# Kernel tuning notes

Measured on AMD Instinct MI355X. Metric: run time of the kernel, lower is better.

## Reference

```python
import jax, jax.numpy as jnp
import numpy as np

DIM = 128
BITS = 4
LEVELS_HALF = 2 ** (BITS - 1)  # 8
# MSE-optimal uniform quantizer step constant for a unit-mean-abs Laplace source,
# 4-bit (16 levels). (TurboQuantMSE dist='laplace')
LAPLACE_STEP_C = 0.456
EPS = 1e-8
SQRT_DIM = float(np.sqrt(DIM))


def fwht(x):
    """Normalized fast Walsh-Hadamard transform over the last dim (power of 2)."""
    n = x.shape[-1]
    orig = x.shape
    y = x
    h = 1
    while h < n:
        y = y.reshape(orig[:-1] + (n // (2 * h), 2, h))
        a, b = y[..., 0, :], y[..., 1, :]
        y = jnp.stack([a + b, a - b], axis=-2).reshape(orig)
        h *= 2
    return y * (1.0 / np.sqrt(n))


def setup_inputs() -> dict:
    key = jax.random.key(0)
    k1, k2 = jax.random.split(key)
    x = jax.random.normal(k1, (4, 32, 4096, DIM), dtype=jnp.float32)
    signs = jax.random.uniform(k2, (1, DIM), dtype=jnp.float32)  # thresholded to +/-1 inside reference
    return {"x": x, "signs": signs}


def reference(x, signs):
    # random-sign Hadamard rotation passes
    s = jnp.where(signs >= 0.5, 1.0, -1.0).astype(x.dtype)  # [P, D]
    n_passes = s.shape[0]
    r = x
    for p in range(n_passes):
        r = fwht(r * s[p])
    # per-vector norm, unit-RMS normalize
    norms = jnp.sqrt(jnp.sum(r * r, axis=-1, keepdims=True))          # [..., 1]
    u = r / (norms + EPS) * SQRT_DIM                                   # unit-RMS coeffs
    # MSE-optimal Laplace step (per-vector scale)
    scales = LAPLACE_STEP_C * jnp.mean(jnp.abs(u), axis=-1, keepdims=True)  # [..., 1]
    q = jnp.clip(jnp.round(u / (scales + EPS)), -LEVELS_HALF, LEVELS_HALF - 1)
    code = (q + LEVELS_HALF).astype(jnp.uint8)                         # [0, 15]
    # pack: two 4-bit codes per byte
    packed = code[..., 0::2] | (code[..., 1::2] << 4)                  # [..., D//2] uint8
    # ---- dequantize ----
    lo = (packed & 0xF).astype(x.dtype) - LEVELS_HALF
    hi = (packed >> 4).astype(x.dtype) - LEVELS_HALF
    qd = jnp.stack([lo, hi], axis=-1).reshape(packed.shape[:-1] + (DIM,))
    r_hat = qd * scales * (norms / SQRT_DIM)
    x_hat = r_hat
    for p in range(n_passes - 1, -1, -1):
        x_hat = fwht(x_hat) * s[p]   # inverse of (H . diag(s)) is diag(s) . H (H symmetric orthonormal)
    return x_hat
```

## Files before the change

kernel.cpp:

```cpp
#include <hip/hip_runtime.h>
#include <math.h>


#define DIM 128
#define INV_SQRT_DIM 0.08838834764831845f

template <int M>
__device__ __forceinline__ float swz_xor(float v) {
    int r = __builtin_amdgcn_ds_swizzle(__float_as_int(v), (M << 10) | 0x1F);
    return __int_as_float(r);
}

__device__ __forceinline__ float sflip(float v, unsigned sbits, int k) {
    unsigned m = ((sbits >> k) & 1u) << 31;
    return __int_as_float(__float_as_int(v) ^ m);
}

__device__ __forceinline__ void fwht_raw(float a[16], int lane) {
#pragma unroll
    for (int h = 1; h < 16; h <<= 1) {
#pragma unroll
        for (int i = 0; i < 16; ++i) {
            if (!(i & h)) {
                float u = a[i], w = a[i + h];
                a[i] = u + w;
                a[i + h] = u - w;
            }
        }
    }
    {
        const float sgn = (lane & 1) ? -1.0f : 1.0f;
#pragma unroll
        for (int i = 0; i < 16; ++i) { float b = swz_xor<1>(a[i]); a[i] = fmaf(sgn, a[i], b); }
    }
    {
        const float sgn = (lane & 2) ? -1.0f : 1.0f;
#pragma unroll
        for (int i = 0; i < 16; ++i) { float b = swz_xor<2>(a[i]); a[i] = fmaf(sgn, a[i], b); }
    }
    {
        const float sgn = (lane & 4) ? -1.0f : 1.0f;
#pragma unroll
        for (int i = 0; i < 16; ++i) { float b = swz_xor<4>(a[i]); a[i] = fmaf(sgn, a[i], b); }
    }
}

__global__ __launch_bounds__(256) void turboquant_kernel(
    const float* __restrict__ x, const float* __restrict__ signs,
    float* __restrict__ out, long long nrows) {
    const int lane = threadIdx.x & 63;
    const int j    = lane & 7;
    const int rsub = lane >> 3;

    unsigned sbits = 0;
#pragma unroll
    for (int k = 0; k < 4; ++k) {
        float4 sv = *reinterpret_cast<const float4*>(signs + k * 32 + j * 4);
        if (sv.x < 0.5f) sbits |= 1u << (k * 4 + 0);
        if (sv.y < 0.5f) sbits |= 1u << (k * 4 + 1);
        if (sv.z < 0.5f) sbits |= 1u << (k * 4 + 2);
        if (sv.w < 0.5f) sbits |= 1u << (k * 4 + 3);
    }

    const long long waves_total = (long long)gridDim.x * 4;
    const long long wid = (long long)blockIdx.x * 4 + (threadIdx.x >> 6);

    for (long long it = wid; it * 8 < nrows; it += waves_total) {
        const long long row = it * 8 + rsub;
        const float* rp = x + row * DIM + j * 4;

        float a[16];
#pragma unroll
        for (int k = 0; k < 4; ++k) {
            float4 v = *reinterpret_cast<const float4*>(rp + k * 32);
            a[k * 4 + 0] = sflip(v.x, sbits, k * 4 + 0);
            a[k * 4 + 1] = sflip(v.y, sbits, k * 4 + 1);
            a[k * 4 + 2] = sflip(v.z, sbits, k * 4 + 2);
            a[k * 4 + 3] = sflip(v.w, sbits, k * 4 + 3);
        }

        fwht_raw(a, lane);

        float ss = 0.0f, sa = 0.0f;
#pragma unroll
        for (int i = 0; i < 16; ++i) {
            ss = fmaf(a[i], a[i], ss);
            sa += fabsf(a[i]);
        }
        ss += swz_xor<1>(ss); sa += swz_xor<1>(sa);
        ss += swz_xor<2>(ss); sa += swz_xor<2>(sa);
        ss += swz_xor<4>(ss); sa += swz_xor<4>(sa);

        const float norm   = sqrtf(ss) * INV_SQRT_DIM;
        const float t      = norm + 1e-8f;
        const float scales = (0.456f / 128.0f) * sa / t;
        const float sden   = scales + 1e-8f;
        const float id     = 1.0f / (t * sden);
        const float ofac   = scales * norm * (1.0f / 128.0f);

#pragma unroll
        for (int i = 0; i < 16; ++i)
            a[i] = fminf(fmaxf(rintf(a[i] * id), -8.0f), 7.0f);

        fwht_raw(a, lane);

        float* op = out + row * DIM + j * 4;
#pragma unroll
        for (int k = 0; k < 4; ++k) {
            float4 o;
            o.x = sflip(a[k * 4 + 0] * ofac, sbits, k * 4 + 0);
            o.y = sflip(a[k * 4 + 1] * ofac, sbits, k * 4 + 1);
            o.z = sflip(a[k * 4 + 2] * ofac, sbits, k * 4 + 2);
            o.w = sflip(a[k * 4 + 3] * ofac, sbits, k * 4 + 3);
            *reinterpret_cast<float4*>(op + k * 32) = o;
        }
    }
}

extern "C" void kernel_launch(void* const* d_in, const int* in_sizes, int n_in,
                              void* d_out, int out_size, void* d_ws, size_t ws_size,
                              hipStream_t stream) {
    const float* x     = (const float*)d_in[0];
    const float* signs = (const float*)d_in[1];
    float* out = (float*)d_out;
    const long long nrows = (long long)in_sizes[0] / DIM;
    turboquant_kernel<<<2048, 256, 0, stream>>>(x, signs, out, nrows);
}
```

Baseline: 106.0 us.

## Prefetch next row tile in registers and use DPP for xor-1/xor-2 shuffles

Each wave now loads the next tile's input into registers before processing the current one, so global load latency overlaps with the FWHT and quantization math. The lane-xor exchanges at distances 1 and 2 move from ds_swizzle to DPP quad_perm moves, which skip the LDS crossbar path. The cost is extra VGPRs for the prefetch buffer, which may lower occupancy. The kernel is memory-bound at about 16M rows, so the overall gain is likely small.

```diff
diff --git a/kernel.cpp b/kernel.cpp
--- a/kernel.cpp
+++ b/kernel.cpp
@@ -5,9 +5,14 @@
 #define DIM 128
 #define INV_SQRT_DIM 0.08838834764831845f
 
-template <int M>
-__device__ __forceinline__ float swz_xor(float v) {
-    int r = __builtin_amdgcn_ds_swizzle(__float_as_int(v), (M << 10) | 0x1F);
+__device__ __forceinline__ float dpp_xor1(float v) {
+    return __int_as_float(__builtin_amdgcn_mov_dpp(__float_as_int(v), 0xB1, 0xF, 0xF, false));
+}
+__device__ __forceinline__ float dpp_xor2(float v) {
+    return __int_as_float(__builtin_amdgcn_mov_dpp(__float_as_int(v), 0x4E, 0xF, 0xF, false));
+}
+__device__ __forceinline__ float swz_xor4(float v) {
+    int r = __builtin_amdgcn_ds_swizzle(__float_as_int(v), (4 << 10) | 0x1F);
     return __int_as_float(r);
 }
 
@@ -31,17 +36,17 @@
     {
         const float sgn = (lane & 1) ? -1.0f : 1.0f;
 #pragma unroll
-        for (int i = 0; i < 16; ++i) { float b = swz_xor<1>(a[i]); a[i] = fmaf(sgn, a[i], b); }
+        for (int i = 0; i < 16; ++i) { float b = dpp_xor1(a[i]); a[i] = fmaf(sgn, a[i], b); }
     }
     {
         const float sgn = (lane & 2) ? -1.0f : 1.0f;
 #pragma unroll
-        for (int i = 0; i < 16; ++i) { float b = swz_xor<2>(a[i]); a[i] = fmaf(sgn, a[i], b); }
+        for (int i = 0; i < 16; ++i) { float b = dpp_xor2(a[i]); a[i] = fmaf(sgn, a[i], b); }
     }
     {
         const float sgn = (lane & 4) ? -1.0f : 1.0f;
 #pragma unroll
-        for (int i = 0; i < 16; ++i) { float b = swz_xor<4>(a[i]); a[i] = fmaf(sgn, a[i], b); }
+        for (int i = 0; i < 16; ++i) { float b = swz_xor4(a[i]); a[i] = fmaf(sgn, a[i], b); }
     }
 }
 
@@ -62,21 +67,35 @@
         if (sv.w < 0.5f) sbits |= 1u << (k * 4 + 3);
     }
 
+    const long long ntiles = nrows >> 3;
     const long long waves_total = (long long)gridDim.x * 4;
-    const long long wid = (long long)blockIdx.x * 4 + (threadIdx.x >> 6);
+    long long t = (long long)blockIdx.x * 4 + (threadIdx.x >> 6);
 
-    for (long long it = wid; it * 8 < nrows; it += waves_total) {
-        const long long row = it * 8 + rsub;
-        const float* rp = x + row * DIM + j * 4;
+    const long long lofs = (long long)rsub * DIM + j * 4;
+
+    float4 cur[4];
+    if (t < ntiles) {
+        const float* rp = x + t * (8 * DIM) + lofs;
+#pragma unroll
+        for (int k = 0; k < 4; ++k) cur[k] = *reinterpret_cast<const float4*>(rp + k * 32);
+    }
+
+    while (t < ntiles) {
+        const long long tn = t + waves_total;
+        float4 nxt[4] = {};
+        if (tn < ntiles) {
+            const float* rp = x + tn * (8 * DIM) + lofs;
+#pragma unroll
+            for (int k = 0; k < 4; ++k) nxt[k] = *reinterpret_cast<const float4*>(rp + k * 32);
+        }
 
         float a[16];
 #pragma unroll
         for (int k = 0; k < 4; ++k) {
-            float4 v = *reinterpret_cast<const float4*>(rp + k * 32);
-            a[k * 4 + 0] = sflip(v.x, sbits, k * 4 + 0);
-            a[k * 4 + 1] = sflip(v.y, sbits, k * 4 + 1);
-            a[k * 4 + 2] = sflip(v.z, sbits, k * 4 + 2);
-            a[k * 4 + 3] = sflip(v.w, sbits, k * 4 + 3);
+            a[k * 4 + 0] = sflip(cur[k].x, sbits, k * 4 + 0);
+            a[k * 4 + 1] = sflip(cur[k].y, sbits, k * 4 + 1);
+            a[k * 4 + 2] = sflip(cur[k].z, sbits, k * 4 + 2);
+            a[k * 4 + 3] = sflip(cur[k].w, sbits, k * 4 + 3);
         }
 
         fwht_raw(a, lane);
@@ -87,15 +106,15 @@
             ss = fmaf(a[i], a[i], ss);
             sa += fabsf(a[i]);
         }
-        ss += swz_xor<1>(ss); sa += swz_xor<1>(sa);
-        ss += swz_xor<2>(ss); sa += swz_xor<2>(sa);
-        ss += swz_xor<4>(ss); sa += swz_xor<4>(sa);
+        ss += dpp_xor1(ss); sa += dpp_xor1(sa);
+        ss += dpp_xor2(ss); sa += dpp_xor2(sa);
+        ss += swz_xor4(ss); sa += swz_xor4(sa);
 
         const float norm   = sqrtf(ss) * INV_SQRT_DIM;
-        const float t      = norm + 1e-8f;
-        const float scales = (0.456f / 128.0f) * sa / t;
+        const float tt     = norm + 1e-8f;
+        const float scales = (0.456f / 128.0f) * sa / tt;
         const float sden   = scales + 1e-8f;
-        const float id     = 1.0f / (t * sden);
+        const float id     = 1.0f / (tt * sden);
         const float ofac   = scales * norm * (1.0f / 128.0f);
 
 #pragma unroll
@@ -104,7 +123,7 @@
 
         fwht_raw(a, lane);
 
-        float* op = out + row * DIM + j * 4;
+        float* op = out + t * (8 * DIM) + lofs;
 #pragma unroll
         for (int k = 0; k < 4; ++k) {
             float4 o;
@@ -114,6 +133,10 @@
             o.w = sflip(a[k * 4 + 3] * ofac, sbits, k * 4 + 3);
             *reinterpret_cast<float4*>(op + k * 32) = o;
         }
+
+        t = tn;
+#pragma unroll
+        for (int k = 0; k < 4; ++k) cur[k] = nxt[k];
     }
 }
 
```

After: 103.0 us. -2.8%, faster.
